# Kernel optimization log

Measured on AMD Instinct MI355X. Metric: run time of the kernel, lower is better.

Reference implementation:

```python
import jax, jax.numpy as jnp
import numpy as np
import math

B, T, D = 2, 2048, 1024
H = 16
HD = D // H
DFF = 4096
EPS = 1e-5


def setup_inputs() -> dict:
    key = jax.random.key(0)
    ks = jax.random.split(key, 11)
    s = 0.02
    return {
        "x": jax.random.normal(ks[0], (B, T, D), dtype=jnp.float32),
        "scale1": jnp.ones((D,), jnp.float32),
        "scale2": jnp.ones((D,), jnp.float32),
        "Wqkv": jax.random.normal(ks[1], (D, 3 * D), jnp.float32) * s,
        "bqkv": jnp.zeros((3 * D,), jnp.float32),
        "Wo": jax.random.normal(ks[2], (D, D), jnp.float32) * s,
        "bo": jnp.zeros((D,), jnp.float32),
        "W1": jax.random.normal(ks[3], (D, DFF), jnp.float32) * s,
        "b1": jnp.zeros((DFF,), jnp.float32),
        "W2": jax.random.normal(ks[4], (DFF, D), jnp.float32) * s,
        "b2": jnp.zeros((D,), jnp.float32),
    }


def rmsnorm(x, scale):
    # Faithful to source: norm = ||x||/sqrt(d); out = scale * x / (norm + eps)
    d = x.shape[-1]
    norm = jnp.linalg.norm(x, axis=-1, keepdims=True) * (1.0 / math.sqrt(d))
    return scale * x / (norm + EPS)


def attention(x, Wqkv, bqkv, Wo, bo):
    b, t, c = x.shape
    qkv = x @ Wqkv + bqkv                       # [B,T,3D]
    qkv = qkv.reshape(b, t, 3, H, HD)
    q, k, v = qkv[:, :, 0], qkv[:, :, 1], qkv[:, :, 2]   # [B,T,H,HD]
    scores = jnp.einsum("bqhd,bkhd->bhqk", q, k) / math.sqrt(HD)
    w = jax.nn.softmax(scores, axis=-1)
    out = jnp.einsum("bhqk,bkhd->bqhd", w, v).reshape(b, t, c)
    return out @ Wo + bo


def reference(x, scale1, scale2, Wqkv, bqkv, Wo, bo, W1, b1, W2, b2):
    x = x + attention(rmsnorm(x, scale1), Wqkv, bqkv, Wo, bo)
    h = rmsnorm(x, scale2)
    ff = (jax.nn.gelu(h @ W1 + b1, approximate=False)) @ W2 + b2
    return x + ff
```

## Files before the change

### kernel.cpp

```cpp
#include <hip/hip_runtime.h>
#include <hip/hip_bf16.h>
#include <math.h>

typedef unsigned short u16;
typedef __bf16 bf16x8 __attribute__((ext_vector_type(8)));
typedef float f32x4 __attribute__((ext_vector_type(4)));
typedef unsigned int u32x2 __attribute__((ext_vector_type(2)));

#define B_   2
#define T_   2048
#define D_   1024
#define H_   16
#define HD_  64
#define DFF_ 4096
#define M_TOK (B_*T_)

__device__ __forceinline__ u16 f2bf(float f){
  unsigned u = __float_as_uint(f);
  u += 0x7fff + ((u>>16)&1);
  return (u16)(u>>16);
}
__device__ __forceinline__ float bflo(unsigned u){ return __uint_as_float(u<<16); }
__device__ __forceinline__ float bfhi(unsigned u){ return __uint_as_float(u & 0xffff0000u); }

__device__ __forceinline__ void gl2lds16(const void* g, void* l){
  __builtin_amdgcn_global_load_lds((const __attribute__((address_space(1))) void*)g,
                                   (__attribute__((address_space(3))) void*)l, 16, 0, 0);
}

__device__ __forceinline__ unsigned lds_u32(const void* p){
  return (unsigned)(uintptr_t)(const __attribute__((address_space(3))) void*)p;
}

__device__ __forceinline__ u32x2 tr_read(unsigned addr){
  u32x2 d;
  asm volatile("ds_read_b64_tr_b16 %0, %1" : "=v"(d) : "v"(addr));
  return d;
}
__device__ __forceinline__ u32x2 tr_read512(unsigned addr){
  u32x2 d;
  asm volatile("ds_read_b64_tr_b16 %0, %1 offset:512" : "=v"(d) : "v"(addr));
  return d;
}
__device__ __forceinline__ bf16x8 pack8(u32x2 a, u32x2 b){
  union { u32x2 u[2]; bf16x8 v; } x; x.u[0]=a; x.u[1]=b; return x.v;
}
__device__ __forceinline__ unsigned cvt_pk_bf16(float a, float b){
  unsigned r;
  asm("v_cvt_pk_bf16_f32 %0, %1, %2" : "=v"(r) : "v"(a), "v"(b));
  return r;
}

__device__ __forceinline__ void block_barrier(){
  asm volatile("" ::: "memory");
  __builtin_amdgcn_s_barrier();
  __builtin_amdgcn_sched_barrier(0);
  asm volatile("" ::: "memory");
}

__device__ __forceinline__ int xcd_chunk(int orig, int nwg){
  int q = nwg >> 3, r = nwg & 7;
  int x = orig & 7, s = orig >> 3;
  return (x < r ? x*(q+1) : r*(q+1) + (x-r)*q) + s;
}

__device__ __forceinline__ void transpose_tile(const float* __restrict__ in, u16* __restrict__ out,
                                               int K, int N, int bxi, int byi, int tid){
  __shared__ float t[32][33];
  int bx = bxi*32, by = byi*32;
  int tx = tid&31, ty = tid>>5;
  #pragma unroll
  for(int i=ty;i<32;i+=8) t[i][tx] = in[(size_t)(by+i)*N + bx + tx];
  __syncthreads();
  #pragma unroll
  for(int i=ty;i<32;i+=8) out[(size_t)(bx+i)*K + by + tx] = f2bf(t[tx][i]);
}

__global__ __launch_bounds__(256) void k_prep(const float* __restrict__ Wqkv, u16* __restrict__ Wqkvt,
                                              const float* __restrict__ Wo,   u16* __restrict__ Wot,
                                              const float* __restrict__ W1,   u16* __restrict__ W1t,
                                              const float* __restrict__ W2,   u16* __restrict__ W2t,
                                              const float* __restrict__ x, const float* __restrict__ scale1,
                                              u16* __restrict__ xn1){
  const int blk = blockIdx.x;
  const int tid = threadIdx.x;
  if(blk < 3072){
    transpose_tile(Wqkv, Wqkvt, D_, 3*D_, blk%96, blk/96, tid);
  } else if(blk < 4096){
    int lb = blk - 3072;
    transpose_tile(Wo, Wot, D_, D_, lb%32, lb/32, tid);
  } else if(blk < 8192){
    int lb = blk - 4096;
    transpose_tile(W1, W1t, D_, DFF_, lb%128, lb/128, tid);
  } else if(blk < 12288){
    int lb = blk - 8192;
    transpose_tile(W2, W2t, DFF_, D_, lb%32, lb/32, tid);
  } else {
    int row = blk - 12288;
    int lane = tid&63, wave = tid>>6;
    const float4* xr = (const float4*)(x + (size_t)row*D_);
    float4 v = xr[tid];
    float ss = v.x*v.x + v.y*v.y + v.z*v.z + v.w*v.w;
    #pragma unroll
    for(int o=1;o<64;o<<=1) ss += __shfl_xor(ss, o);
    __shared__ float red[4];
    if(lane==0) red[wave]=ss;
    __syncthreads();
    float tot = red[0]+red[1]+red[2]+red[3];
    float inv = 1.0f/(sqrtf(tot*(1.0f/D_)) + 1e-5f);
    float4 s4 = ((const float4*)scale1)[tid];
    u16* o4 = xn1 + (size_t)row*D_ + tid*4;
    o4[0]=f2bf(v.x*s4.x*inv); o4[1]=f2bf(v.y*s4.y*inv);
    o4[2]=f2bf(v.z*s4.z*inv); o4[3]=f2bf(v.w*s4.w*inv);
  }
}

template<int EPI>
__global__ __launch_bounds__(512,2) void k_gemm256(const u16* __restrict__ A, const u16* __restrict__ Bt,
                                                   const float* __restrict__ bias,
                                                   void* __restrict__ Cout, int M, int N, int K,
                                                   int nbx, int nby, int splitk){
  __shared__ u16 LDS[4][16384];
  const int tid = threadIdx.x;
  const int lane = tid&63, wave = tid>>6;
  const int lo = lane&15, hi = lane>>4;
  const int wm = wave>>2, wn = wave&3;
  const int l = xcd_chunk(blockIdx.x, gridDim.x);
  const int row0 = (l % nbx)*256;
  const int col0 = ((l / nbx) % nby)*256;
  const int kc   = l / (nbx*nby);
  const int klen = K/splitk, kbeg = kc*klen;
  f32x4 acc[8][4];
  #pragma unroll
  for(int m=0;m<8;m++)
    #pragma unroll
    for(int n=0;n<4;n++) acc[m][n] = (f32x4){0.f,0.f,0.f,0.f};
  const u16* Ag = A + (size_t)row0*K + kbeg;
  const u16* Bg = Bt + (size_t)col0*K + kbeg;
  const int NT = klen>>5;

  const int cc0 = tid, cc1 = tid+512;
  const size_t s0 = (size_t)(cc0>>2)*K + (size_t)((((cc0&3)^((cc0>>3)&3)))<<3);
  const size_t s1 = (size_t)(cc1>>2)*K + (size_t)((((cc1&3)^((cc1>>3)&3)))<<3);

  #define STAGE_A(t) { const u16* Ab = Ag + (size_t)(t)*32; char* d = (char*)LDS[(t)&3]; \
    gl2lds16(Ab + s0, d + cc0*16); gl2lds16(Ab + s1, d + cc1*16); }
  #define STAGE_B(t) { const u16* Bb = Bg + (size_t)(t)*32; char* d = (char*)LDS[(t)&3] + 16384; \
    gl2lds16(Bb + s0, d + cc0*16); gl2lds16(Bb + s1, d + cc1*16); }

  STAGE_A(0); STAGE_B(0); STAGE_A(1); STAGE_B(1); STAGE_A(2); STAGE_B(2);

  const unsigned slot = (unsigned)((hi ^ ((lo>>1)&3))<<4);
  for(int t=0;t<NT;t++){
    if(t<NT-2)       { asm volatile("s_waitcnt vmcnt(8)" ::: "memory"); }
    else if(t==NT-2) { asm volatile("s_waitcnt vmcnt(4)" ::: "memory"); }
    else             { asm volatile("s_waitcnt vmcnt(0)" ::: "memory"); }
    block_barrier();
    const char* bufp = (const char*)LDS[t&3];
    const char* ap = bufp + (wm*128 + lo)*64 + slot;
    const char* bp = bufp + 16384 + (wn*64 + lo)*64 + slot;

    if(t+3<NT) STAGE_A(t+3);
    __builtin_amdgcn_sched_barrier(0);
    bf16x8 a0[4], b[4];
    #pragma unroll
    for(int m=0;m<4;m++) a0[m] = *(const bf16x8*)(ap + m*1024);
    #pragma unroll
    for(int n=0;n<4;n++) b[n]  = *(const bf16x8*)(bp + n*1024);
    __builtin_amdgcn_s_setprio(1);
    #pragma unroll
    for(int m=0;m<4;m++)
      #pragma unroll
      for(int n=0;n<4;n++)
        acc[m][n] = __builtin_amdgcn_mfma_f32_16x16x32_bf16(a0[m], b[n], acc[m][n], 0,0,0);
    __builtin_amdgcn_s_setprio(0);

    if(t+3<NT) STAGE_B(t+3);
    __builtin_amdgcn_sched_barrier(0);
    bf16x8 a1[4];
    #pragma unroll
    for(int m=0;m<4;m++) a1[m] = *(const bf16x8*)(ap + 4096 + m*1024);
    __builtin_amdgcn_s_setprio(1);
    #pragma unroll
    for(int m=0;m<4;m++)
      #pragma unroll
      for(int n=0;n<4;n++)
        acc[m+4][n] = __builtin_amdgcn_mfma_f32_16x16x32_bf16(a1[m], b[n], acc[m+4][n], 0,0,0);
    __builtin_amdgcn_s_setprio(0);
  }
  #undef STAGE_A
  #undef STAGE_B

  u16* Pk = (u16*)Cout + (size_t)kc*M*N;
  #pragma unroll
  for(int m=0;m<8;m++){
    #pragma unroll
    for(int n=0;n<4;n++){
      #pragma unroll
      for(int r=0;r<4;r++){
        int row = row0 + wm*128 + m*16 + hi*4 + r;
        int col = col0 + wn*64 + n*16 + lo;
        if constexpr(EPI==3){
          Pk[(size_t)row*N + col] = f2bf(acc[m][n][r]);
        } else {
          float v = acc[m][n][r] + bias[col];
          if constexpr(EPI==2){
            v = 0.5f*v*(1.0f + erff(v*0.70710678118f));
          }
          ((u16*)Cout)[(size_t)row*N + col] = f2bf(v);
        }
      }
    }
  }
}

__global__ __launch_bounds__(256) void k_ff2_reduce4(const u16* __restrict__ P,
                                                     const float* __restrict__ bias,
                                                     const float* __restrict__ res,
                                                     float* __restrict__ out){
  const size_t stride8 = (size_t)M_TOK*D_/8;
  size_t idx = (size_t)blockIdx.x*256 + threadIdx.x;
  const uint4* p = (const uint4*)P;
  uint4 q0 = p[idx], q1 = p[idx+stride8], q2 = p[idx+2*stride8], q3 = p[idx+3*stride8];
  size_t base = idx*8;
  const float4* rr = (const float4*)(res + base);
  const float4* bb = (const float4*)(bias + (base & (D_-1)));
  float4 r0 = rr[0], r1 = rr[1];
  float4 b0 = bb[0], b1 = bb[1];
  float4 o0, o1;
  unsigned w;
  w=q0.x; o0.x  = bflo(w); o0.y  = bfhi(w);
  w=q0.y; o0.z  = bflo(w); o0.w  = bfhi(w);
  w=q0.z; o1.x  = bflo(w); o1.y  = bfhi(w);
  w=q0.w; o1.z  = bflo(w); o1.w  = bfhi(w);
  w=q1.x; o0.x += bflo(w); o0.y += bfhi(w);
  w=q1.y; o0.z += bflo(w); o0.w += bfhi(w);
  w=q1.z; o1.x += bflo(w); o1.y += bfhi(w);
  w=q1.w; o1.z += bflo(w); o1.w += bfhi(w);
  w=q2.x; o0.x += bflo(w); o0.y += bfhi(w);
  w=q2.y; o0.z += bflo(w); o0.w += bfhi(w);
  w=q2.z; o1.x += bflo(w); o1.y += bfhi(w);
  w=q2.w; o1.z += bflo(w); o1.w += bfhi(w);
  w=q3.x; o0.x += bflo(w); o0.y += bfhi(w);
  w=q3.y; o0.z += bflo(w); o0.w += bfhi(w);
  w=q3.z; o1.x += bflo(w); o1.y += bfhi(w);
  w=q3.w; o1.z += bflo(w); o1.w += bfhi(w);
  o0.x += b0.x + r0.x; o0.y += b0.y + r0.y; o0.z += b0.z + r0.z; o0.w += b0.w + r0.w;
  o1.x += b1.x + r1.x; o1.y += b1.y + r1.y; o1.z += b1.z + r1.z; o1.w += b1.w + r1.w;
  float4* oo = (float4*)(out + base);
  oo[0] = o0; oo[1] = o1;
}

__global__ __launch_bounds__(256) void k_wo_reduce_rms(const u16* __restrict__ P,
                                                       const float* __restrict__ bo,
                                                       const float* __restrict__ x,
                                                       const float* __restrict__ scale2,
                                                       float* __restrict__ x2,
                                                       u16* __restrict__ xn2){
  int row = blockIdx.x;
  int tid = threadIdx.x;
  int lane = tid&63, wave = tid>>6;
  const size_t stride = (size_t)M_TOK*D_;
  const u16* pr = P + (size_t)row*D_;
  uint2 a0 = ((const uint2*)pr)[tid];
  uint2 a1 = ((const uint2*)(pr + stride))[tid];
  uint2 a2 = ((const uint2*)(pr + 2*stride))[tid];
  uint2 a3 = ((const uint2*)(pr + 3*stride))[tid];
  float4 r = ((const float4*)(x + (size_t)row*D_))[tid];
  float4 bi = ((const float4*)bo)[tid];
  float4 v;
  v.x = bflo(a0.x)+bflo(a1.x)+bflo(a2.x)+bflo(a3.x) + bi.x + r.x;
  v.y = bfhi(a0.x)+bfhi(a1.x)+bfhi(a2.x)+bfhi(a3.x) + bi.y + r.y;
  v.z = bflo(a0.y)+bflo(a1.y)+bflo(a2.y)+bflo(a3.y) + bi.z + r.z;
  v.w = bfhi(a0.y)+bfhi(a1.y)+bfhi(a2.y)+bfhi(a3.y) + bi.w + r.w;
  ((float4*)(x2 + (size_t)row*D_))[tid] = v;
  float ss = v.x*v.x + v.y*v.y + v.z*v.z + v.w*v.w;
  #pragma unroll
  for(int o=1;o<64;o<<=1) ss += __shfl_xor(ss, o);
  __shared__ float red[4];
  if(lane==0) red[wave]=ss;
  __syncthreads();
  float tot = red[0]+red[1]+red[2]+red[3];
  float inv = 1.0f/(sqrtf(tot*(1.0f/D_)) + 1e-5f);
  float4 s4 = ((const float4*)scale2)[tid];
  u16* o4 = xn2 + (size_t)row*D_ + tid*4;
  o4[0]=f2bf(v.x*s4.x*inv); o4[1]=f2bf(v.y*s4.y*inv);
  o4[2]=f2bf(v.z*s4.z*inv); o4[3]=f2bf(v.w*s4.w*inv);
}

__global__ __launch_bounds__(512,4) void k_attn(const u16* __restrict__ qkv, u16* __restrict__ O){
  __shared__ alignas(16) u16 Ks[2][4096];
  __shared__ alignas(16) u16 Vs[2][4096];
  __shared__ alignas(16) u16 Ps[8][1024];
  const int l = xcd_chunk(blockIdx.x, 512);
  const int qt = l & 15, bh = l >> 4;
  const int h = bh & 15, b = bh >> 4;
  const int tid = threadIdx.x, lane = tid&63, wave = tid>>6;
  const int lo = lane&15, hi = lane>>4, l7 = lane&7;
  const u16* qkvB = qkv + (size_t)b*T_*3072;
  const int hoff = h*64;
  const float C2 = 0.18033688f;

  const int q0 = qt*128 + wave*16;
  const u16* qp = qkvB + (size_t)(q0+lo)*3072 + hoff + hi*8;
  bf16x8 aq0 = *(const bf16x8*)qp;
  bf16x8 aq1 = *(const bf16x8*)(qp+32);

  size_t sK, sV;
  {
    int c = tid;
    sK = (size_t)(c>>3)*3072 + 1024 + hoff + (((c&7)^((c>>3)&7))<<3);
    int kv = ((c>>5)<<2) + ((c>>1)&3);
    int d0 = (((c&31)>>3)<<4) | ((c&1)<<3);
    sV = (size_t)kv*3072 + 2048 + hoff + d0;
  }
  const unsigned kb0 = (unsigned)lo*128 + (unsigned)((hi^l7))*16;
  const unsigned kb1 = (unsigned)lo*128 + (unsigned)(((hi|4)^l7))*16;
  const unsigned vtr = (unsigned)hi*1024 + (unsigned)lo*2;
  const unsigned swzQ = (unsigned)(lo&7)<<4;

  f32x4 oac[4];
  #pragma unroll
  for(int n=0;n<4;n++) oac[n] = (f32x4){0.f,0.f,0.f,0.f};
  float mrow = -1e30f;
  float lsum = 0.f;

  {
    gl2lds16(qkvB + sK, (char*)Ks[0] + tid*16);
    gl2lds16(qkvB + sV, (char*)Vs[0] + tid*16);
  }
  int buf = 0;
  for(int t=0;t<T_/64;t++){
    __syncthreads();
    if(t < T_/64-1){
      size_t koff = (size_t)(t+1)*64*3072;
      gl2lds16(qkvB + koff + sK, (char*)Ks[buf^1] + tid*16);
      gl2lds16(qkvB + koff + sV, (char*)Vs[buf^1] + tid*16);
    }
    const char* K_ = (const char*)Ks[buf];
    u16* P_ = Ps[wave];

    f32x4 s[4];
    __builtin_amdgcn_s_setprio(1);
    #pragma unroll
    for(int n=0;n<4;n++){
      bf16x8 k0f = *(const bf16x8*)(K_ + n*2048 + kb0);
      bf16x8 k1f = *(const bf16x8*)(K_ + n*2048 + kb1);
      f32x4 z = (f32x4){0.f,0.f,0.f,0.f};
      z = __builtin_amdgcn_mfma_f32_16x16x32_bf16(k0f, aq0, z, 0,0,0);
      z = __builtin_amdgcn_mfma_f32_16x16x32_bf16(k1f, aq1, z, 0,0,0);
      s[n] = z;
    }
    __builtin_amdgcn_s_setprio(0);

    float mx = s[0][0];
    #pragma unroll
    for(int n=0;n<4;n++)
      #pragma unroll
      for(int r=0;r<4;r++) mx = fmaxf(mx, s[n][r]);

    if(!__all(mx <= mrow + 64.0f)){
      float mm = fmaxf(mx, __shfl_xor(mx,16));
      mm = fmaxf(mm, __shfl_xor(mm,32));
      float nm = fmaxf(mrow, mm);
      float alpha = exp2f((mrow - nm)*C2);
      mrow = nm;
      lsum *= alpha;
      float ar[4];
      #pragma unroll
      for(int r=0;r<4;r++) ar[r] = __shfl(alpha, hi*4 + r);
      #pragma unroll
      for(int n=0;n<4;n++)
        #pragma unroll
        for(int r=0;r<4;r++) oac[n][r] *= ar[r];
    }

    const float nmC2 = -mrow*C2;
    #pragma unroll
    for(int n=0;n<4;n++){
      float p0v = exp2f(fmaf(s[n][0], C2, nmC2));
      float p1v = exp2f(fmaf(s[n][1], C2, nmC2));
      float p2v = exp2f(fmaf(s[n][2], C2, nmC2));
      float p3v = exp2f(fmaf(s[n][3], C2, nmC2));
      lsum += (p0v+p1v)+(p2v+p3v);
      u32x2 pw;
      pw[0] = cvt_pk_bf16(p0v, p1v);
      pw[1] = cvt_pk_bf16(p2v, p3v);
      *(u32x2*)((char*)P_ + (unsigned)lo*128 + (((unsigned)(n*32 + hi*8)) ^ swzQ)) = pw;
    }

    const unsigned vsb = lds_u32(Vs[buf]);
    #pragma unroll
    for(int kk=0;kk<2;kk++){
      bf16x8 ap = *(const bf16x8*)((const char*)P_ + (kk==0 ? kb0 : kb1));
      u32x2 t0[4], t1[4];
      #pragma unroll
      for(int n=0;n<4;n++){
        unsigned a = vsb + vtr + (unsigned)kk*4096 + (unsigned)n*128;
        t0[n] = tr_read(a);
        t1[n] = tr_read512(a);
      }
      asm volatile("s_waitcnt lgkmcnt(0)" ::: "memory");
      __builtin_amdgcn_sched_barrier(0);
      __builtin_amdgcn_s_setprio(1);
      #pragma unroll
      for(int n=0;n<4;n++){
        bf16x8 bv = pack8(t0[n], t1[n]);
        oac[n] = __builtin_amdgcn_mfma_f32_16x16x32_bf16(ap, bv, oac[n], 0,0,0);
      }
      __builtin_amdgcn_s_setprio(0);
    }
    buf ^= 1;
  }

  lsum += __shfl_xor(lsum, 16);
  lsum += __shfl_xor(lsum, 32);
  float linv = 1.0f/lsum;
  float lr[4];
  #pragma unroll
  for(int r=0;r<4;r++) lr[r] = __shfl(linv, hi*4 + r);
  size_t obase = ((size_t)b*T_ + q0)*D_ + hoff;
  #pragma unroll
  for(int n=0;n<4;n++)
    #pragma unroll
    for(int r=0;r<4;r++)
      O[obase + (size_t)(hi*4+r)*D_ + n*16 + lo] = f2bf(oac[n][r]*lr[r]);
}

extern "C" void kernel_launch(void* const* d_in, const int* in_sizes, int n_in,
                              void* d_out, int out_size, void* d_ws, size_t ws_size,
                              hipStream_t stream){
  (void)in_sizes; (void)n_in; (void)out_size; (void)ws_size;
  const float* x      = (const float*)d_in[0];
  const float* scale1 = (const float*)d_in[1];
  const float* scale2 = (const float*)d_in[2];
  const float* Wqkv   = (const float*)d_in[3];
  const float* bqkv   = (const float*)d_in[4];
  const float* Wo     = (const float*)d_in[5];
  const float* bo     = (const float*)d_in[6];
  const float* W1     = (const float*)d_in[7];
  const float* b1     = (const float*)d_in[8];
  const float* W2     = (const float*)d_in[9];
  const float* b2     = (const float*)d_in[10];
  float* out = (float*)d_out;

  char* w = (char*)d_ws;
  u16* xn1   = (u16*)w;  w += (size_t)M_TOK*D_*2;
  u16* qkvb  = (u16*)w;  w += (size_t)M_TOK*3*D_*2;
  u16* Obuf  = (u16*)w;  w += (size_t)M_TOK*D_*2;
  float* x2  = (float*)w; w += (size_t)M_TOK*D_*4;
  u16* xn2   = (u16*)w;  w += (size_t)M_TOK*D_*2;
  u16* h1    = (u16*)w;  w += (size_t)M_TOK*DFF_*2;
  u16* Wqkvt = (u16*)w;  w += (size_t)3*D_*D_*2;
  u16* Wot   = (u16*)w;  w += (size_t)D_*D_*2;
  u16* W1t   = (u16*)w;  w += (size_t)D_*DFF_*2;
  u16* W2t   = (u16*)w;  w += (size_t)DFF_*D_*2;
  u16* wop = (u16*)d_ws;
  u16* pkb = (u16*)d_ws;

  k_prep<<<16384, 256, 0, stream>>>(Wqkv, Wqkvt, Wo, Wot, W1, W1t, W2, W2t, x, scale1, xn1);
  k_gemm256<0><<<192, 512, 0, stream>>>(xn1, Wqkvt, bqkv, qkvb, M_TOK, 3*D_, D_, M_TOK/256, 3*D_/256, 1);
  k_attn<<<512, 512, 0, stream>>>(qkvb, Obuf);
  k_gemm256<3><<<256, 512, 0, stream>>>(Obuf, Wot, nullptr, wop, M_TOK, D_, D_, M_TOK/256, D_/256, 4);
  k_wo_reduce_rms<<<M_TOK, 256, 0, stream>>>(wop, bo, x, scale2, x2, xn2);
  k_gemm256<2><<<256, 512, 0, stream>>>(xn2, W1t, b1, h1, M_TOK, DFF_, D_, M_TOK/256, DFF_/256, 1);
  k_gemm256<3><<<256, 512, 0, stream>>>(h1, W2t, nullptr, pkb, M_TOK, D_, DFF_, M_TOK/256, D_/256, 4);
  k_ff2_reduce4<<<2048, 256, 0, stream>>>(pkb, b2, x2, out);
}
```

Baseline: 251.5 us.

## Overlap Wo/W1/W2 weight transposes with the QKV GEMM in one launch

The Wo, W1 and W2 transpose-to-bf16 work moves out of the prep kernel into a combined kernel. Its first 192 blocks run the QKV GEMM and the remaining blocks each transpose two 32x32 tiles. The aim is to fill idle CUs during the 192-block GEMM, which cannot occupy the whole GPU, and to shrink the prep kernel. The risk is that transpose blocks compete with GEMM blocks for bandwidth and CU slots, and the block scheduler may not interleave them usefully since the GEMM blocks are dispatched first.

```diff
diff --git a/kernel.cpp b/kernel.cpp
--- a/kernel.cpp
+++ b/kernel.cpp
@@ -64,11 +64,11 @@
   return (x < r ? x*(q+1) : r*(q+1) + (x-r)*q) + s;
 }
 
-__device__ __forceinline__ void transpose_tile(const float* __restrict__ in, u16* __restrict__ out,
-                                               int K, int N, int bxi, int byi, int tid){
-  __shared__ float t[32][33];
+__device__ __forceinline__ void transpose_tile_b(float (*t)[33],
+                                                 const float* __restrict__ in, u16* __restrict__ out,
+                                                 int K, int N, int bxi, int byi, int tid256){
   int bx = bxi*32, by = byi*32;
-  int tx = tid&31, ty = tid>>5;
+  int tx = tid256&31, ty = tid256>>5;
   #pragma unroll
   for(int i=ty;i<32;i+=8) t[i][tx] = in[(size_t)(by+i)*N + bx + tx];
   __syncthreads();
@@ -77,26 +77,15 @@
 }
 
 __global__ __launch_bounds__(256) void k_prep(const float* __restrict__ Wqkv, u16* __restrict__ Wqkvt,
-                                              const float* __restrict__ Wo,   u16* __restrict__ Wot,
-                                              const float* __restrict__ W1,   u16* __restrict__ W1t,
-                                              const float* __restrict__ W2,   u16* __restrict__ W2t,
                                               const float* __restrict__ x, const float* __restrict__ scale1,
                                               u16* __restrict__ xn1){
   const int blk = blockIdx.x;
   const int tid = threadIdx.x;
+  __shared__ float tbuf[32][33];
   if(blk < 3072){
-    transpose_tile(Wqkv, Wqkvt, D_, 3*D_, blk%96, blk/96, tid);
-  } else if(blk < 4096){
-    int lb = blk - 3072;
-    transpose_tile(Wo, Wot, D_, D_, lb%32, lb/32, tid);
-  } else if(blk < 8192){
-    int lb = blk - 4096;
-    transpose_tile(W1, W1t, D_, DFF_, lb%128, lb/128, tid);
-  } else if(blk < 12288){
-    int lb = blk - 8192;
-    transpose_tile(W2, W2t, DFF_, D_, lb%32, lb/32, tid);
+    transpose_tile_b(tbuf, Wqkv, Wqkvt, D_, 3*D_, blk%96, blk/96, tid);
   } else {
-    int row = blk - 12288;
+    int row = blk - 3072;
     int lane = tid&63, wave = tid>>6;
     const float4* xr = (const float4*)(x + (size_t)row*D_);
     float4 v = xr[tid];
@@ -112,6 +101,112 @@
     u16* o4 = xn1 + (size_t)row*D_ + tid*4;
     o4[0]=f2bf(v.x*s4.x*inv); o4[1]=f2bf(v.y*s4.y*inv);
     o4[2]=f2bf(v.z*s4.z*inv); o4[3]=f2bf(v.w*s4.w*inv);
+  }
+}
+
+__global__ __launch_bounds__(512,2) void k_qkv_prep2(const u16* __restrict__ A, const u16* __restrict__ Bt,
+                                                     const float* __restrict__ bias, u16* __restrict__ Cout,
+                                                     const float* __restrict__ Wo, u16* __restrict__ Wot,
+                                                     const float* __restrict__ W1, u16* __restrict__ W1t,
+                                                     const float* __restrict__ W2, u16* __restrict__ W2t){
+  __shared__ u16 LDS[4][16384];
+  const int tid = threadIdx.x;
+  if(blockIdx.x >= 192){
+    float (*tp)[33] = (float(*)[33])((char*)LDS + (tid>>8)*(32*33*4 + 64));
+    int tile = (blockIdx.x - 192)*2 + (tid>>8);
+    int tid256 = tid & 255;
+    if(tile < 1024){
+      transpose_tile_b(tp, Wo, Wot, D_, D_, tile%32, tile/32, tid256);
+    } else if(tile < 5120){
+      int t2 = tile - 1024;
+      transpose_tile_b(tp, W1, W1t, D_, DFF_, t2%128, t2/128, tid256);
+    } else {
+      int t2 = tile - 5120;
+      transpose_tile_b(tp, W2, W2t, DFF_, D_, t2%32, t2/32, tid256);
+    }
+    return;
+  }
+  const int M = M_TOK, N = 3*D_, K = D_;
+  const int lane = tid&63, wave = tid>>6;
+  const int lo = lane&15, hi = lane>>4;
+  const int wm = wave>>2, wn = wave&3;
+  const int l = xcd_chunk(blockIdx.x, 192);
+  const int nbx = M_TOK/256;
+  const int row0 = (l % nbx)*256;
+  const int col0 = (l / nbx)*256;
+  f32x4 acc[8][4];
+  #pragma unroll
+  for(int m=0;m<8;m++)
+    #pragma unroll
+    for(int n=0;n<4;n++) acc[m][n] = (f32x4){0.f,0.f,0.f,0.f};
+  const u16* Ag = A + (size_t)row0*K;
+  const u16* Bg = Bt + (size_t)col0*K;
+  const int NT = K>>5;
+
+  const int cc0 = tid, cc1 = tid+512;
+  const size_t s0 = (size_t)(cc0>>2)*K + (size_t)((((cc0&3)^((cc0>>3)&3)))<<3);
+  const size_t s1 = (size_t)(cc1>>2)*K + (size_t)((((cc1&3)^((cc1>>3)&3)))<<3);
+
+  #define STAGE_A(t) { const u16* Ab = Ag + (size_t)(t)*32; char* d = (char*)LDS[(t)&3]; \
+    gl2lds16(Ab + s0, d + cc0*16); gl2lds16(Ab + s1, d + cc1*16); }
+  #define STAGE_B(t) { const u16* Bb = Bg + (size_t)(t)*32; char* d = (char*)LDS[(t)&3] + 16384; \
+    gl2lds16(Bb + s0, d + cc0*16); gl2lds16(Bb + s1, d + cc1*16); }
+
+  STAGE_A(0); STAGE_B(0); STAGE_A(1); STAGE_B(1); STAGE_A(2); STAGE_B(2);
+
+  const unsigned slot = (unsigned)((hi ^ ((lo>>1)&3))<<4);
+  for(int t=0;t<NT;t++){
+    if(t<NT-2)       { asm volatile("s_waitcnt vmcnt(8)" ::: "memory"); }
+    else if(t==NT-2) { asm volatile("s_waitcnt vmcnt(4)" ::: "memory"); }
+    else             { asm volatile("s_waitcnt vmcnt(0)" ::: "memory"); }
+    block_barrier();
+    const char* bufp = (const char*)LDS[t&3];
+    const char* ap = bufp + (wm*128 + lo)*64 + slot;
+    const char* bp = bufp + 16384 + (wn*64 + lo)*64 + slot;
+
+    if(t+3<NT) STAGE_A(t+3);
+    __builtin_amdgcn_sched_barrier(0);
+    bf16x8 a0[4], b[4];
+    #pragma unroll
+    for(int m=0;m<4;m++) a0[m] = *(const bf16x8*)(ap + m*1024);
+    #pragma unroll
+    for(int n=0;n<4;n++) b[n]  = *(const bf16x8*)(bp + n*1024);
+    __builtin_amdgcn_s_setprio(1);
+    #pragma unroll
+    for(int m=0;m<4;m++)
+      #pragma unroll
+      for(int n=0;n<4;n++)
+        acc[m][n] = __builtin_amdgcn_mfma_f32_16x16x32_bf16(a0[m], b[n], acc[m][n], 0,0,0);
+    __builtin_amdgcn_s_setprio(0);
+
+    if(t+3<NT) STAGE_B(t+3);
+    __builtin_amdgcn_sched_barrier(0);
+    bf16x8 a1[4];
+    #pragma unroll
+    for(int m=0;m<4;m++) a1[m] = *(const bf16x8*)(ap + 4096 + m*1024);
+    __builtin_amdgcn_s_setprio(1);
+    #pragma unroll
+    for(int m=0;m<4;m++)
+      #pragma unroll
+      for(int n=0;n<4;n++)
+        acc[m+4][n] = __builtin_amdgcn_mfma_f32_16x16x32_bf16(a1[m], b[n], acc[m+4][n], 0,0,0);
+    __builtin_amdgcn_s_setprio(0);
+  }
+  #undef STAGE_A
+  #undef STAGE_B
+
+  #pragma unroll
+  for(int m=0;m<8;m++){
+    #pragma unroll
+    for(int n=0;n<4;n++){
+      #pragma unroll
+      for(int r=0;r<4;r++){
+        int row = row0 + wm*128 + m*16 + hi*4 + r;
+        int col = col0 + wn*64 + n*16 + lo;
+        float v = acc[m][n][r] + bias[col];
+        Cout[(size_t)row*N + col] = f2bf(v);
+      }
+    }
   }
 }
 
@@ -458,8 +553,8 @@
   u16* wop = (u16*)d_ws;
   u16* pkb = (u16*)d_ws;
 
-  k_prep<<<16384, 256, 0, stream>>>(Wqkv, Wqkvt, Wo, Wot, W1, W1t, W2, W2t, x, scale1, xn1);
-  k_gemm256<0><<<192, 512, 0, stream>>>(xn1, Wqkvt, bqkv, qkvb, M_TOK, 3*D_, D_, M_TOK/256, 3*D_/256, 1);
+  k_prep<<<7168, 256, 0, stream>>>(Wqkv, Wqkvt, x, scale1, xn1);
+  k_qkv_prep2<<<4800, 512, 0, stream>>>(xn1, Wqkvt, bqkv, qkvb, Wo, Wot, W1, W1t, W2, W2t);
   k_attn<<<512, 512, 0, stream>>>(qkvb, Obuf);
   k_gemm256<3><<<256, 512, 0, stream>>>(Obuf, Wot, nullptr, wop, M_TOK, D_, D_, M_TOK/256, D_/256, 4);
   k_wo_reduce_rms<<<M_TOK, 256, 0, stream>>>(wop, bo, x, scale2, x2, xn2);
```

After: 249.5 us. About the same (-0.8%).
